# Performance work log

Measured on AMD Instinct MI355X. Metric: run time of the kernel, lower is better.

The kernel has to match this reference:

```python
import jax, jax.numpy as jnp
import numpy as np

N_NODES = 20000
N_EDGES = 320000
L = 512   # input feature dim (size_dict['small'][0])
D = 256   # hidden dim (feat_channel), heads=1 so head_dim = 256
C = 2     # n_classes


def setup_inputs() -> dict:
    key = jax.random.key(0)
    ks = jax.random.split(key, 18)
    s = 0.02
    inp = {
        "x": jax.random.normal(ks[0], (N_NODES, L), jnp.float32),
        "edge_index": jax.random.randint(ks[1], (2, N_EDGES), 0, N_NODES, dtype=jnp.int32),
        "label": 1,
        # TransformerConv(L, D, heads=1): query/key/value + root skip projections
        "Wq": jax.random.normal(ks[2], (L, D), jnp.float32) * s,
        "bq": jax.random.normal(ks[3], (D,), jnp.float32) * s,
        "Wk": jax.random.normal(ks[4], (L, D), jnp.float32) * s,
        "bk": jax.random.normal(ks[5], (D,), jnp.float32) * s,
        "Wv": jax.random.normal(ks[6], (L, D), jnp.float32) * s,
        "bv": jax.random.normal(ks[7], (D,), jnp.float32) * s,
        "Ws": jax.random.normal(ks[8], (L, D), jnp.float32) * s,
        "bs": jax.random.normal(ks[9], (D,), jnp.float32) * s,
        # GlobalAdaptPooling: tanh-MLP attention (heads = n_classes) + per-class classifier
        "Wa1": jax.random.normal(ks[10], (D, D), jnp.float32) * s,
        "ba1": jax.random.normal(ks[11], (D,), jnp.float32) * s,
        "Wa2": jax.random.normal(ks[12], (D, C), jnp.float32) * s,
        "ba2": jax.random.normal(ks[13], (C,), jnp.float32) * s,
        "Wc": jax.random.normal(ks[14], (C, D), jnp.float32) * s,
        "bc": jax.random.normal(ks[15], (C,), jnp.float32) * s,
    }
    return inp


def _forward(x, edge_index, label, Wq, bq, Wk, bk, Wv, bv, Ws, bs, Wa1, ba1, Wa2, ba2, Wc, bc):
    n = x.shape[0]
    src = edge_index[0]  # message source j
    dst = edge_index[1]  # message target i
    # --- TransformerConv (heads=1, concat, root_weight=True) ---
    q = x @ Wq + bq                      # [N, D]
    k = x @ Wk + bk
    v = x @ Wv + bv
    score = jnp.sum(q[dst] * k[src], axis=-1) / jnp.sqrt(jnp.float32(D))  # [E]
    # segment softmax over incoming edges of each target node
    m = jax.ops.segment_max(score, dst, num_segments=n)
    e = jnp.exp(score - m[dst])
    den = jax.ops.segment_sum(e, dst, num_segments=n)
    alpha = e / den[dst]                 # [E]
    agg = jax.ops.segment_sum(alpha[:, None] * v[src], dst, num_segments=n)  # [N, D]
    h = agg + x @ Ws + bs
    # --- act: GELU (torch exact/erf) ---
    h = jax.nn.gelu(h, approximate=False)
    # --- GlobalAdaptPooling: node attention with n_classes heads ---
    scores = jnp.tanh(h @ Wa1 + ba1) @ Wa2 + ba2      # [N, C]
    attn = jax.nn.softmax(scores, axis=0)             # softmax over nodes
    M = attn.T @ h                                    # [C, D] per-class bag embedding
    logits = (jnp.sum(M * Wc, axis=1) + bc)[None, :]  # [1, C]
    Y_prob = jax.nn.softmax(logits, axis=1)
    A = attn[:, label]                                # [N] attention for target class
    return logits, Y_prob, A


def reference(x, edge_index, label, Wq, bq, Wk, bk, Wv, bv, Ws, bs, Wa1, ba1, Wa2, ba2, Wc, bc):
    return _forward(x, edge_index, label, Wq, bq, Wk, bk, Wv, bv, Ws, bs, Wa1, ba1, Wa2, ba2, Wc, bc)
```

## Files before the change

kernel.cpp:

```cpp
#include <hip/hip_runtime.h>
#include <hip/hip_bf16.h>
#include <math.h>

typedef float f32x4_t __attribute__((ext_vector_type(4)));
typedef float f32x2_t __attribute__((ext_vector_type(2)));
typedef __bf16 bf16x8_t __attribute__((ext_vector_type(8)));

__device__ __forceinline__ float bf2f(unsigned int u){
  union { float f; unsigned int i; } x; x.i = u << 16; return x.f;
}
__device__ __forceinline__ unsigned short f2bf(float f){
  unsigned int x = __float_as_uint(f);
  unsigned int r = (x + 0x7fffu + ((x >> 16) & 1u)) >> 16;
  return (unsigned short)r;
}
__device__ __forceinline__ void unp8s(uint4 w, float* f, float s){
  f[0] = bf2f(w.x & 0xffffu) * s; f[1] = bf2f(w.x >> 16) * s;
  f[2] = bf2f(w.y & 0xffffu) * s; f[3] = bf2f(w.y >> 16) * s;
  f[4] = bf2f(w.z & 0xffffu) * s; f[5] = bf2f(w.z >> 16) * s;
  f[6] = bf2f(w.w & 0xffffu) * s; f[7] = bf2f(w.w >> 16) * s;
}
__device__ __forceinline__ void unpf8(unsigned int w, float* f){
  f32x2_t lo = __builtin_amdgcn_cvt_pk_f32_fp8(w, false);
  f32x2_t hi = __builtin_amdgcn_cvt_pk_f32_fp8(w, true);
  f[0] = lo[0]; f[1] = lo[1]; f[2] = hi[0]; f[3] = hi[1];
}

#define GLOAD16(gsrc, ldst) \
  __builtin_amdgcn_global_load_lds((const __attribute__((address_space(1))) unsigned int*)(gsrc), \
                                   (__attribute__((address_space(3))) unsigned int*)(ldst), 16, 0, 0)

__global__ void pack_weights(const float* __restrict__ Wq, const float* __restrict__ Wk,
                             const float* __restrict__ Wv, const float* __restrict__ Ws,
                             const float* __restrict__ bq, const float* __restrict__ bk,
                             const float* __restrict__ bv, const float* __restrict__ bs,
                             unsigned short* __restrict__ wcatT, float* __restrict__ bcat){
  int idx = blockIdx.x * 256 + threadIdx.x;
  if (idx < 1024 * 512){
    int c = idx >> 9, k = idx & 511;
    int sel = c >> 8, cc = c & 255;
    const float* W = (sel == 0) ? Wq : (sel == 1) ? Wk : (sel == 2) ? Wv : Ws;
    wcatT[idx] = f2bf(W[k * 256 + cc]);
  }
  if (idx < 1024){
    int sel = idx >> 8, cc = idx & 255;
    const float* B = (sel == 0) ? bq : (sel == 1) ? bk : (sel == 2) ? bv : bs;
    bcat[idx] = B[cc];
  }
}

__global__ void pack_wa1(const float* __restrict__ Wa1, unsigned short* __restrict__ wa1T){
  int idx = blockIdx.x * 256 + threadIdx.x;
  int c = idx >> 8, k = idx & 255;
  wa1T[idx] = f2bf(Wa1[k * 256 + c]);
}

__global__ void convert_x(const float* __restrict__ x, unsigned short* __restrict__ xbf, int n4){
  int i = blockIdx.x * 256 + threadIdx.x;
  if (i < n4){
    float4 v = reinterpret_cast<const float4*>(x)[i];
    ushort4 o;
    o.x = f2bf(v.x); o.y = f2bf(v.y); o.z = f2bf(v.z); o.w = f2bf(v.w);
    reinterpret_cast<ushort4*>(xbf)[i] = o;
  }
}

__global__ __launch_bounds__(256) void gemm_qkvs(const unsigned short* __restrict__ xbf,
                                                 const unsigned short* __restrict__ wcatT,
                                                 const float* __restrict__ bcat,
                                                 unsigned short* __restrict__ qkvs, int n_nodes){
  __shared__ __align__(16) unsigned short As[128 * 32];
  __shared__ __align__(16) unsigned short Bs[128 * 32];
  const int tid = threadIdx.x;
  const int lane = tid & 63, wave = tid >> 6;
  const int wm = wave >> 1, wn = wave & 1;
  const int m0 = blockIdx.y * 128, n0 = blockIdx.x * 128;
  const int lrow = lane >> 2;
  const int lcol = (lane & 3) * 8;
  const int rA0 = min(m0 + wave * 16 + lrow, n_nodes - 1);
  const int rA1 = min(m0 + (wave + 4) * 16 + lrow, n_nodes - 1);
  const int rB0 = n0 + wave * 16 + lrow;
  const int rB1 = n0 + (wave + 4) * 16 + lrow;
  const int r = lane & 15, ko = (lane >> 4) * 8;
  f32x4_t acc[4][4] = {};
  for (int k0 = 0; k0 < 512; k0 += 32){
    GLOAD16(xbf   + (size_t)rA0 * 512 + k0 + lcol, &As[wave * 512]);
    GLOAD16(xbf   + (size_t)rA1 * 512 + k0 + lcol, &As[(wave + 4) * 512]);
    GLOAD16(wcatT + (size_t)rB0 * 512 + k0 + lcol, &Bs[wave * 512]);
    GLOAD16(wcatT + (size_t)rB1 * 512 + k0 + lcol, &Bs[(wave + 4) * 512]);
    __syncthreads();
    bf16x8_t a[4], b[4];
    #pragma unroll
    for (int mi = 0; mi < 4; mi++)
      a[mi] = *reinterpret_cast<const bf16x8_t*>(&As[(wm * 64 + mi * 16 + r) * 32 + ko]);
    #pragma unroll
    for (int ni = 0; ni < 4; ni++)
      b[ni] = *reinterpret_cast<const bf16x8_t*>(&Bs[(wn * 64 + ni * 16 + r) * 32 + ko]);
    #pragma unroll
    for (int mi = 0; mi < 4; mi++)
      #pragma unroll
      for (int ni = 0; ni < 4; ni++)
        acc[mi][ni] = __builtin_amdgcn_mfma_f32_16x16x32_bf16(a[mi], b[ni], acc[mi][ni], 0, 0, 0);
    __syncthreads();
  }
  const int rg = (lane >> 4) * 4;
  #pragma unroll
  for (int ni = 0; ni < 4; ni++){
    int gcol = n0 + wn * 64 + ni * 16 + r;
    float bb = bcat[gcol];
    #pragma unroll
    for (int mi = 0; mi < 4; mi++){
      #pragma unroll
      for (int j = 0; j < 4; j++){
        int grow = m0 + wm * 64 + mi * 16 + rg + j;
        if (grow < n_nodes)
          qkvs[(size_t)grow * 1024 + gcol] = f2bf(acc[mi][ni][j] + bb);
      }
    }
  }
}

__global__ void pack_kv8(const unsigned short* __restrict__ qkvs, unsigned char* __restrict__ kv8, int n){
  int idx = blockIdx.x * 256 + threadIdx.x;
  if (idx >= n * 64) return;
  int node = idx >> 6, part = idx & 63;
  const unsigned short* src = qkvs + (size_t)node * 1024 + 256 + part * 8;
  uint4 w = *reinterpret_cast<const uint4*>(src);
  float f[8]; unp8s(w, f, 1.0f);
  int lo = 0, hi = 0;
  lo = __builtin_amdgcn_cvt_pk_fp8_f32(f[0], f[1], lo, false);
  lo = __builtin_amdgcn_cvt_pk_fp8_f32(f[2], f[3], lo, true);
  hi = __builtin_amdgcn_cvt_pk_fp8_f32(f[4], f[5], hi, false);
  hi = __builtin_amdgcn_cvt_pk_fp8_f32(f[6], f[7], hi, true);
  uint2 o; o.x = (unsigned int)lo; o.y = (unsigned int)hi;
  *reinterpret_cast<uint2*>(kv8 + (size_t)node * 512 + part * 8) = o;
}

__global__ void degree_hist(const int* __restrict__ ei, int* __restrict__ deg, int ne){
  int i = blockIdx.x * 256 + threadIdx.x;
  if (i < ne) atomicAdd(&deg[ei[ne + i]], 1);
}

__global__ void scan_deg(const int* __restrict__ deg, int* __restrict__ rowstart, int n, int ne){
  __shared__ int sm[1024];
  int tid = threadIdx.x;
  int per = (n + 1023) / 1024;
  int start = tid * per;
  int sum = 0;
  for (int i = 0; i < per; i++){
    int idx = start + i;
    sum += (idx < n) ? deg[idx] : 0;
  }
  sm[tid] = sum; __syncthreads();
  for (int off = 1; off < 1024; off <<= 1){
    int t = (tid >= off) ? sm[tid - off] : 0;
    __syncthreads();
    sm[tid] += t;
    __syncthreads();
  }
  int run = sm[tid] - sum;
  for (int i = 0; i < per; i++){
    int idx = start + i;
    if (idx < n){
      rowstart[idx] = run;
      run += deg[idx];
    }
  }
  if (tid == 0) rowstart[n] = ne;
}

__global__ void scatter_edges(const int* __restrict__ ei, const int* __restrict__ rowstart,
                              int* __restrict__ cursor, int* __restrict__ csrsrc, int ne){
  int i = blockIdx.x * 256 + threadIdx.x;
  if (i < ne){
    int d = ei[ne + i];
    int pos = atomicAdd(&cursor[d], 1);
    csrsrc[rowstart[d] + pos] = ei[i] << 9;
  }
}

__global__ __launch_bounds__(256) void edge_attn(const unsigned short* __restrict__ qkvs,
                                                 const unsigned char* __restrict__ kv8,
                                                 const int* __restrict__ rowstart,
                                                 const int* __restrict__ csrsrc,
                                                 unsigned short* __restrict__ hbf, int n_nodes){
  const int tid = threadIdx.x;
  const int lane = tid & 63, wave = tid >> 6;
  const int g = lane >> 4, t = lane & 15;
  const int node = blockIdx.x * 16 + wave * 4 + g;
  const bool active = node < n_nodes;
  const int nd = active ? node : 0;
  const float qs = 0.0625f * 1.44269504088896340736f;
  float q[16];
  {
    const unsigned short* qp = qkvs + (size_t)nd * 1024 + t * 16;
    uint4 w0 = *reinterpret_cast<const uint4*>(qp);
    uint4 w1 = *reinterpret_cast<const uint4*>(qp + 8);
    unp8s(w0, q, qs); unp8s(w1, q + 8, qs);
  }
  int rs = rowstart[nd];
  int re = active ? rowstart[nd + 1] : rs;
  float m = -1e30f, den = 0.f;
  float acc[16];
  #pragma unroll
  for (int j = 0; j < 16; j++) acc[j] = 0.f;
  for (int i = rs; i < re; i++){
    int soff = csrsrc[i];
    const unsigned char* kb = kv8 + (size_t)soff + t * 16;
    uint4 kw = *reinterpret_cast<const uint4*>(kb);
    float kf[16];
    unpf8(kw.x, kf); unpf8(kw.y, kf + 4); unpf8(kw.z, kf + 8); unpf8(kw.w, kf + 12);
    float s = 0.f;
    #pragma unroll
    for (int j = 0; j < 16; j++) s = fmaf(q[j], kf[j], s);
    s += __shfl_xor(s, 1); s += __shfl_xor(s, 2);
    s += __shfl_xor(s, 4); s += __shfl_xor(s, 8);
    uint4 vw = *reinterpret_cast<const uint4*>(kb + 256);
    float vf[16];
    unpf8(vw.x, vf); unpf8(vw.y, vf + 4); unpf8(vw.z, vf + 8); unpf8(vw.w, vf + 12);
    if (s > m){
      float sc = exp2f(m - s);
      den = den * sc + 1.0f;
      #pragma unroll
      for (int j = 0; j < 16; j++) acc[j] = fmaf(acc[j], sc, vf[j]);
      m = s;
    } else {
      float e = exp2f(s - m);
      den += e;
      #pragma unroll
      for (int j = 0; j < 16; j++) acc[j] = fmaf(e, vf[j], acc[j]);
    }
  }
  float inv = (den > 0.f) ? 1.f / den : 0.f;
  const unsigned short* sp = qkvs + (size_t)nd * 1024 + 768 + t * 16;
  uint4 s0 = *reinterpret_cast<const uint4*>(sp);
  uint4 s1 = *reinterpret_cast<const uint4*>(sp + 8);
  float sf[16]; unp8s(s0, sf, 1.0f); unp8s(s1, sf + 8, 1.0f);
  const float inv_sqrt2 = 0.70710678118654752f;
  unsigned int o[8];
  #pragma unroll
  for (int j = 0; j < 8; j++){
    float h0 = acc[2 * j] * inv + sf[2 * j];
    float h1 = acc[2 * j + 1] * inv + sf[2 * j + 1];
    h0 = 0.5f * h0 * (1.f + erff(h0 * inv_sqrt2));
    h1 = 0.5f * h1 * (1.f + erff(h1 * inv_sqrt2));
    o[j] = (unsigned int)f2bf(h0) | ((unsigned int)f2bf(h1) << 16);
  }
  if (active){
    uint4* dst = reinterpret_cast<uint4*>(hbf + (size_t)node * 256 + t * 16);
    dst[0] = make_uint4(o[0], o[1], o[2], o[3]);
    dst[1] = make_uint4(o[4], o[5], o[6], o[7]);
  }
}

__global__ __launch_bounds__(256) void mlp_mfma(const unsigned short* __restrict__ hbf,
                                                const unsigned short* __restrict__ wa1T,
                                                const float* __restrict__ ba1,
                                                const float* __restrict__ Wa2,
                                                const float* __restrict__ ba2,
                                                float* __restrict__ s2, int n_nodes){
  __shared__ __align__(16) unsigned short As[64 * 72];
  __shared__ float s2s[64][2];
  const int tid = threadIdx.x;
  const int lane = tid & 63, wave = tid >> 6;
  const int m0 = blockIdx.x * 64;
  const int c0 = wave * 64;
  const int r = lane & 15, rg = (lane >> 4) * 4;
  if (tid < 128) s2s[tid >> 1][tid & 1] = 0.f;
  f32x4_t acc[4][4] = {};
  for (int k0 = 0; k0 < 256; k0 += 64){
    int arow = tid >> 2, akc = (tid & 3) * 16;
    uint4 a0v = make_uint4(0,0,0,0), a1v = make_uint4(0,0,0,0);
    if (m0 + arow < n_nodes){
      const unsigned short* src = hbf + (size_t)(m0 + arow) * 256 + k0 + akc;
      a0v = *reinterpret_cast<const uint4*>(src);
      a1v = *reinterpret_cast<const uint4*>(src + 8);
    }
    *reinterpret_cast<uint4*>(&As[arow * 72 + akc]) = a0v;
    *reinterpret_cast<uint4*>(&As[arow * 72 + akc + 8]) = a1v;
    __syncthreads();
    #pragma unroll
    for (int kk = 0; kk < 2; kk++){
      int kg = kk * 32 + (lane >> 4) * 8;
      bf16x8_t a[4], b[4];
      #pragma unroll
      for (int mi = 0; mi < 4; mi++)
        a[mi] = *reinterpret_cast<const bf16x8_t*>(&As[(mi * 16 + r) * 72 + kg]);
      #pragma unroll
      for (int ni = 0; ni < 4; ni++)
        b[ni] = *reinterpret_cast<const bf16x8_t*>(wa1T + (size_t)(c0 + ni * 16 + r) * 256 + k0 + kg);
      #pragma unroll
      for (int mi = 0; mi < 4; mi++)
        #pragma unroll
        for (int ni = 0; ni < 4; ni++)
          acc[mi][ni] = __builtin_amdgcn_mfma_f32_16x16x32_bf16(a[mi], b[ni], acc[mi][ni], 0, 0, 0);
    }
    __syncthreads();
  }
  float w20[4], w21[4], b1c[4];
  #pragma unroll
  for (int ni = 0; ni < 4; ni++){
    int col = c0 + ni * 16 + r;
    w20[ni] = Wa2[col * 2]; w21[ni] = Wa2[col * 2 + 1]; b1c[ni] = ba1[col];
  }
  #pragma unroll
  for (int mi = 0; mi < 4; mi++){
    #pragma unroll
    for (int j = 0; j < 4; j++){
      float t0 = 0.f, t1 = 0.f;
      #pragma unroll
      for (int ni = 0; ni < 4; ni++){
        float t = tanhf(acc[mi][ni][j] + b1c[ni]);
        t0 += t * w20[ni]; t1 += t * w21[ni];
      }
      t0 += __shfl_xor(t0, 1); t0 += __shfl_xor(t0, 2);
      t0 += __shfl_xor(t0, 4); t0 += __shfl_xor(t0, 8);
      t1 += __shfl_xor(t1, 1); t1 += __shfl_xor(t1, 2);
      t1 += __shfl_xor(t1, 4); t1 += __shfl_xor(t1, 8);
      if (r == 0){
        int row = mi * 16 + rg + j;
        atomicAdd(&s2s[row][0], t0);
        atomicAdd(&s2s[row][1], t1);
      }
    }
  }
  __syncthreads();
  if (tid < 128){
    int row = tid >> 1, c = tid & 1;
    int node = m0 + row;
    if (node < n_nodes) s2[node * 2 + c] = s2s[row][c] + ba2[c];
  }
}

__global__ void col_reduce(const float* __restrict__ s2, float* __restrict__ red, int n){
  __shared__ float sm[1024];
  __shared__ float mshare[2];
  int tid = threadIdx.x;
  float mx0 = -INFINITY, mx1 = -INFINITY;
  for (int i = tid; i < n; i += 1024){
    mx0 = fmaxf(mx0, s2[2 * i]);
    mx1 = fmaxf(mx1, s2[2 * i + 1]);
  }
  sm[tid] = mx0; __syncthreads();
  for (int off = 512; off > 0; off >>= 1){
    if (tid < off) sm[tid] = fmaxf(sm[tid], sm[tid + off]);
    __syncthreads();
  }
  if (tid == 0) mshare[0] = sm[0];
  __syncthreads();
  sm[tid] = mx1; __syncthreads();
  for (int off = 512; off > 0; off >>= 1){
    if (tid < off) sm[tid] = fmaxf(sm[tid], sm[tid + off]);
    __syncthreads();
  }
  if (tid == 0) mshare[1] = sm[0];
  __syncthreads();
  float m0 = mshare[0], m1 = mshare[1];
  float s0 = 0.f, s1 = 0.f;
  for (int i = tid; i < n; i += 1024){
    s0 += expf(s2[2 * i] - m0);
    s1 += expf(s2[2 * i + 1] - m1);
  }
  sm[tid] = s0; __syncthreads();
  for (int off = 512; off > 0; off >>= 1){
    if (tid < off) sm[tid] += sm[tid + off];
    __syncthreads();
  }
  float den0 = sm[0];
  __syncthreads();
  sm[tid] = s1; __syncthreads();
  for (int off = 512; off > 0; off >>= 1){
    if (tid < off) sm[tid] += sm[tid + off];
    __syncthreads();
  }
  if (tid == 0){
    red[0] = m0; red[1] = m1; red[2] = den0; red[3] = sm[0];
  }
}

__global__ __launch_bounds__(256) void attn_M(const float* __restrict__ s2, const float* __restrict__ red,
                                              const unsigned short* __restrict__ hbf, const int* __restrict__ label,
                                              float* __restrict__ Mbuf, float* __restrict__ outA, int n){
  __shared__ float a0s[256], a1s[256];
  int tid = threadIdx.x;
  int n0 = blockIdx.x * 256;
  int node = n0 + tid;
  float m0 = red[0], m1 = red[1];
  float i0 = 1.f / red[2], i1 = 1.f / red[3];
  float a0 = 0.f, a1 = 0.f;
  if (node < n){
    a0 = expf(s2[2 * node] - m0) * i0;
    a1 = expf(s2[2 * node + 1] - m1) * i1;
    outA[node] = (label[0] == 0) ? a0 : a1;
  }
  a0s[tid] = a0; a1s[tid] = a1;
  __syncthreads();
  int d = tid;
  float M0 = 0.f, M1 = 0.f;
  int cnt = min(256, n - n0);
  for (int i = 0; i < cnt; i++){
    float hv = bf2f((unsigned int)hbf[(size_t)(n0 + i) * 256 + d]);
    M0 += a0s[i] * hv;
    M1 += a1s[i] * hv;
  }
  atomicAdd(&Mbuf[d], M0);
  atomicAdd(&Mbuf[256 + d], M1);
}

__global__ void final_k(const float* __restrict__ Mbuf, const float* __restrict__ Wc,
                        const float* __restrict__ bc, float* __restrict__ out){
  __shared__ float sm[256];
  __shared__ float l0s;
  int tid = threadIdx.x;
  float p0 = Mbuf[tid] * Wc[tid];
  float p1 = Mbuf[256 + tid] * Wc[256 + tid];
  sm[tid] = p0; __syncthreads();
  for (int off = 128; off > 0; off >>= 1){
    if (tid < off) sm[tid] += sm[tid + off];
    __syncthreads();
  }
  if (tid == 0) l0s = sm[0];
  __syncthreads();
  sm[tid] = p1; __syncthreads();
  for (int off = 128; off > 0; off >>= 1){
    if (tid < off) sm[tid] += sm[tid + off];
    __syncthreads();
  }
  if (tid == 0){
    float l0 = l0s + bc[0];
    float l1 = sm[0] + bc[1];
    out[0] = l0; out[1] = l1;
    float mx = fmaxf(l0, l1);
    float e0 = expf(l0 - mx), e1 = expf(l1 - mx);
    float inv = 1.f / (e0 + e1);
    out[2] = e0 * inv; out[3] = e1 * inv;
  }
}

extern "C" void kernel_launch(void* const* d_in, const int* in_sizes, int n_in,
                              void* d_out, int out_size, void* d_ws, size_t ws_size,
                              hipStream_t stream) {
  const float* x   = (const float*)d_in[0];
  const int*   ei  = (const int*)d_in[1];
  const int*   lab = (const int*)d_in[2];
  const float* Wq  = (const float*)d_in[3];
  const float* bq  = (const float*)d_in[4];
  const float* Wk  = (const float*)d_in[5];
  const float* bk  = (const float*)d_in[6];
  const float* Wv  = (const float*)d_in[7];
  const float* bv  = (const float*)d_in[8];
  const float* Ws  = (const float*)d_in[9];
  const float* bs  = (const float*)d_in[10];
  const float* Wa1 = (const float*)d_in[11];
  const float* ba1 = (const float*)d_in[12];
  const float* Wa2 = (const float*)d_in[13];
  const float* ba2 = (const float*)d_in[14];
  const float* Wc  = (const float*)d_in[15];
  const float* bc  = (const float*)d_in[16];
  float* out = (float*)d_out;

  const int n  = in_sizes[0] / 512;
  const int ne = in_sizes[1] / 2;

  char* ws = (char*)d_ws;
  size_t off = 0;
  auto take = [&](size_t bytes){ size_t r = off; off += (bytes + 255) & ~(size_t)255; return r; };
  unsigned short* xbf    = (unsigned short*)(ws + take((size_t)n * 512 * 2));
  unsigned short* wcatT  = (unsigned short*)(ws + take((size_t)1024 * 512 * 2));
  float*          bcat   = (float*)(ws + take(1024 * 4));
  unsigned short* qkvs   = (unsigned short*)(ws + take((size_t)n * 1024 * 2));
  unsigned char*  kv8    = (unsigned char*)(ws + take((size_t)n * 512));
  unsigned short* hbf    = (unsigned short*)(ws + take((size_t)n * 256 * 2));
  unsigned short* wa1T   = (unsigned short*)(ws + take((size_t)256 * 256 * 2));
  float*          s2     = (float*)(ws + take((size_t)n * 2 * 4));
  size_t zoff = off;
  int*            deg    = (int*)(ws + take((size_t)n * 4));
  int*            cursor = (int*)(ws + take((size_t)n * 4));
  float*          Mbuf   = (float*)(ws + take(512 * 4));
  size_t zlen = off - zoff;
  int*            rowst  = (int*)(ws + take((size_t)(n + 1) * 4));
  int*            csrsrc = (int*)(ws + take((size_t)ne * 4));
  float*          red    = (float*)(ws + take(4 * 4));

  hipMemsetAsync(ws + zoff, 0, zlen, stream);

  pack_weights<<<(1024 * 512 + 255) / 256, 256, 0, stream>>>(Wq, Wk, Wv, Ws, bq, bk, bv, bs, wcatT, bcat);
  pack_wa1<<<256, 256, 0, stream>>>(Wa1, wa1T);
  convert_x<<<(n * 512 / 4 + 255) / 256, 256, 0, stream>>>(x, xbf, n * 512 / 4);
  dim3 ggrid(8, (n + 127) / 128);
  gemm_qkvs<<<ggrid, 256, 0, stream>>>(xbf, wcatT, bcat, qkvs, n);
  pack_kv8<<<(n * 64 + 255) / 256, 256, 0, stream>>>(qkvs, kv8, n);
  degree_hist<<<(ne + 255) / 256, 256, 0, stream>>>(ei, deg, ne);
  scan_deg<<<1, 1024, 0, stream>>>(deg, rowst, n, ne);
  scatter_edges<<<(ne + 255) / 256, 256, 0, stream>>>(ei, rowst, cursor, csrsrc, ne);
  edge_attn<<<(n + 15) / 16, 256, 0, stream>>>(qkvs, kv8, rowst, csrsrc, hbf, n);
  mlp_mfma<<<(n + 63) / 64, 256, 0, stream>>>(hbf, wa1T, ba1, Wa2, ba2, s2, n);
  col_reduce<<<1, 1024, 0, stream>>>(s2, red, n);
  attn_M<<<(n + 255) / 256, 256, 0, stream>>>(s2, red, hbf, lab, Mbuf, out + 4, n);
  final_k<<<1, 256, 0, stream>>>(Mbuf, Wc, bc, out);
  (void)ws_size; (void)out_size; (void)n_in;
}
```

Baseline: 226.2 us.

## Fuse x conversion and KV fp8 packing into QKVS GEMM with staged epilogue

Drops the separate convert_x and pack_kv8 kernels. The GEMM now reads fp32 x, converts it to bf16 in registers and stores it to LDS, and its epilogue writes Q and S as separate bf16 arrays and K/V directly as fp8. Output tiles are staged through shared memory so global stores are coalesced, and the blocks are remapped to a 1D grid with n-block-major grouping. This removes two launches, the xbf round trip and the full qkvs intermediate. In exchange, the A operand is now loaded synchronously through registers instead of via global_load_lds, which could expose more load latency.

```diff
diff --git a/kernel.cpp b/kernel.cpp
--- a/kernel.cpp
+++ b/kernel.cpp
@@ -13,6 +13,9 @@
   unsigned int x = __float_as_uint(f);
   unsigned int r = (x + 0x7fffu + ((x >> 16) & 1u)) >> 16;
   return (unsigned short)r;
+}
+__device__ __forceinline__ unsigned int pk2bf(float a, float b){
+  return (unsigned int)f2bf(a) | ((unsigned int)f2bf(b) << 16);
 }
 __device__ __forceinline__ void unp8s(uint4 w, float* f, float s){
   f[0] = bf2f(w.x & 0xffffu) * s; f[1] = bf2f(w.x >> 16) * s;
@@ -55,39 +58,44 @@
   wa1T[idx] = f2bf(Wa1[k * 256 + c]);
 }
 
-__global__ void convert_x(const float* __restrict__ x, unsigned short* __restrict__ xbf, int n4){
-  int i = blockIdx.x * 256 + threadIdx.x;
-  if (i < n4){
-    float4 v = reinterpret_cast<const float4*>(x)[i];
-    ushort4 o;
-    o.x = f2bf(v.x); o.y = f2bf(v.y); o.z = f2bf(v.z); o.w = f2bf(v.w);
-    reinterpret_cast<ushort4*>(xbf)[i] = o;
-  }
-}
-
-__global__ __launch_bounds__(256) void gemm_qkvs(const unsigned short* __restrict__ xbf,
+__global__ __launch_bounds__(256) void gemm_qkvs(const float* __restrict__ x,
                                                  const unsigned short* __restrict__ wcatT,
                                                  const float* __restrict__ bcat,
-                                                 unsigned short* __restrict__ qkvs, int n_nodes){
-  __shared__ __align__(16) unsigned short As[128 * 32];
-  __shared__ __align__(16) unsigned short Bs[128 * 32];
+                                                 unsigned short* __restrict__ qbf,
+                                                 unsigned short* __restrict__ sbf,
+                                                 unsigned char* __restrict__ kv8,
+                                                 int n_nodes, int mblocks){
+  __shared__ __align__(16) unsigned char smem[128 * 272];
+  unsigned short* As = (unsigned short*)smem;
+  unsigned short* Bs = (unsigned short*)(smem + 8192);
   const int tid = threadIdx.x;
   const int lane = tid & 63, wave = tid >> 6;
   const int wm = wave >> 1, wn = wave & 1;
-  const int m0 = blockIdx.y * 128, n0 = blockIdx.x * 128;
-  const int lrow = lane >> 2;
-  const int lcol = (lane & 3) * 8;
-  const int rA0 = min(m0 + wave * 16 + lrow, n_nodes - 1);
-  const int rA1 = min(m0 + (wave + 4) * 16 + lrow, n_nodes - 1);
-  const int rB0 = n0 + wave * 16 + lrow;
-  const int rB1 = n0 + (wave + 4) * 16 + lrow;
-  const int r = lane & 15, ko = (lane >> 4) * 8;
+  const int g = (blockIdx.x & 7) * mblocks + (blockIdx.x >> 3);
+  const int m_blk = g >> 3, n_blk = g & 7;
+  const int m0 = m_blk * 128, n0 = n_blk * 128;
+  const int arow = tid >> 1;
+  const int acol = (tid & 1) * 16;
+  const float* aptr = x + (size_t)min(m0 + arow, n_nodes - 1) * 512 + acol;
+  unsigned short* adst = &As[arow * 32 + acol];
+  const int brow = n0 + wave * 16 + (lane >> 2);
+  const int bcol = (lane & 3) * 8;
+  const int r = lane & 15, ko = (lane >> 4) * 8, ng = lane >> 4;
   f32x4_t acc[4][4] = {};
   for (int k0 = 0; k0 < 512; k0 += 32){
-    GLOAD16(xbf   + (size_t)rA0 * 512 + k0 + lcol, &As[wave * 512]);
-    GLOAD16(xbf   + (size_t)rA1 * 512 + k0 + lcol, &As[(wave + 4) * 512]);
-    GLOAD16(wcatT + (size_t)rB0 * 512 + k0 + lcol, &Bs[wave * 512]);
-    GLOAD16(wcatT + (size_t)rB1 * 512 + k0 + lcol, &Bs[(wave + 4) * 512]);
+    GLOAD16(wcatT + (size_t)brow * 512 + k0 + bcol, &Bs[wave * 512]);
+    GLOAD16(wcatT + (size_t)(brow + 64) * 512 + k0 + bcol, &Bs[(wave + 4) * 512]);
+    float4 f0 = *reinterpret_cast<const float4*>(aptr + k0);
+    float4 f1 = *reinterpret_cast<const float4*>(aptr + k0 + 4);
+    float4 f2 = *reinterpret_cast<const float4*>(aptr + k0 + 8);
+    float4 f3 = *reinterpret_cast<const float4*>(aptr + k0 + 12);
+    uint4 o0, o1;
+    o0.x = pk2bf(f0.x, f0.y); o0.y = pk2bf(f0.z, f0.w);
+    o0.z = pk2bf(f1.x, f1.y); o0.w = pk2bf(f1.z, f1.w);
+    o1.x = pk2bf(f2.x, f2.y); o1.y = pk2bf(f2.z, f2.w);
+    o1.z = pk2bf(f3.x, f3.y); o1.w = pk2bf(f3.z, f3.w);
+    *reinterpret_cast<uint4*>(adst) = o0;
+    *reinterpret_cast<uint4*>(adst + 8) = o1;
     __syncthreads();
     bf16x8_t a[4], b[4];
     #pragma unroll
@@ -100,40 +108,65 @@
     for (int mi = 0; mi < 4; mi++)
       #pragma unroll
       for (int ni = 0; ni < 4; ni++)
-        acc[mi][ni] = __builtin_amdgcn_mfma_f32_16x16x32_bf16(a[mi], b[ni], acc[mi][ni], 0, 0, 0);
-    __syncthreads();
-  }
-  const int rg = (lane >> 4) * 4;
-  #pragma unroll
-  for (int ni = 0; ni < 4; ni++){
-    int gcol = n0 + wn * 64 + ni * 16 + r;
-    float bb = bcat[gcol];
+        acc[mi][ni] = __builtin_amdgcn_mfma_f32_16x16x32_bf16(b[ni], a[mi], acc[mi][ni], 0, 0, 0);
+    __syncthreads();
+  }
+  const bool isQ = (n_blk < 2), isS = (n_blk >= 6);
+  if (isQ || isS){
+    unsigned short* St = (unsigned short*)smem;
     #pragma unroll
     for (int mi = 0; mi < 4; mi++){
       #pragma unroll
-      for (int j = 0; j < 4; j++){
-        int grow = m0 + wm * 64 + mi * 16 + rg + j;
-        if (grow < n_nodes)
-          qkvs[(size_t)grow * 1024 + gcol] = f2bf(acc[mi][ni][j] + bb);
+      for (int ni = 0; ni < 4; ni++){
+        int ml = wm * 64 + mi * 16 + r;
+        int nl = wn * 64 + ni * 16 + ng * 4;
+        float4 bb = *reinterpret_cast<const float4*>(&bcat[n0 + nl]);
+        uint2 w;
+        w.x = pk2bf(acc[mi][ni][0] + bb.x, acc[mi][ni][1] + bb.y);
+        w.y = pk2bf(acc[mi][ni][2] + bb.z, acc[mi][ni][3] + bb.w);
+        *reinterpret_cast<uint2*>(&St[ml * 136 + nl]) = w;
       }
     }
-  }
-}
-
-__global__ void pack_kv8(const unsigned short* __restrict__ qkvs, unsigned char* __restrict__ kv8, int n){
-  int idx = blockIdx.x * 256 + threadIdx.x;
-  if (idx >= n * 64) return;
-  int node = idx >> 6, part = idx & 63;
-  const unsigned short* src = qkvs + (size_t)node * 1024 + 256 + part * 8;
-  uint4 w = *reinterpret_cast<const uint4*>(src);
-  float f[8]; unp8s(w, f, 1.0f);
-  int lo = 0, hi = 0;
-  lo = __builtin_amdgcn_cvt_pk_fp8_f32(f[0], f[1], lo, false);
-  lo = __builtin_amdgcn_cvt_pk_fp8_f32(f[2], f[3], lo, true);
-  hi = __builtin_amdgcn_cvt_pk_fp8_f32(f[4], f[5], hi, false);
-  hi = __builtin_amdgcn_cvt_pk_fp8_f32(f[6], f[7], hi, true);
-  uint2 o; o.x = (unsigned int)lo; o.y = (unsigned int)hi;
-  *reinterpret_cast<uint2*>(kv8 + (size_t)node * 512 + part * 8) = o;
+    __syncthreads();
+    unsigned short* outp = isQ ? qbf : sbf;
+    const int colhalf = isQ ? n_blk : (n_blk - 6);
+    #pragma unroll
+    for (int it = 0; it < 8; it++){
+      int t = it * 256 + tid;
+      int row = t >> 4, seg = (t & 15) * 8;
+      int node = m0 + row;
+      if (node < n_nodes){
+        uint4 v = *reinterpret_cast<const uint4*>(&St[row * 136 + seg]);
+        *reinterpret_cast<uint4*>(outp + (size_t)node * 256 + colhalf * 128 + seg) = v;
+      }
+    }
+  } else {
+    unsigned char* St = smem;
+    #pragma unroll
+    for (int mi = 0; mi < 4; mi++){
+      #pragma unroll
+      for (int ni = 0; ni < 4; ni++){
+        int ml = wm * 64 + mi * 16 + r;
+        int nl = wn * 64 + ni * 16 + ng * 4;
+        float4 bb = *reinterpret_cast<const float4*>(&bcat[n0 + nl]);
+        int u = 0;
+        u = __builtin_amdgcn_cvt_pk_fp8_f32(acc[mi][ni][0] + bb.x, acc[mi][ni][1] + bb.y, u, false);
+        u = __builtin_amdgcn_cvt_pk_fp8_f32(acc[mi][ni][2] + bb.z, acc[mi][ni][3] + bb.w, u, true);
+        *reinterpret_cast<unsigned int*>(&St[ml * 144 + nl]) = (unsigned int)u;
+      }
+    }
+    __syncthreads();
+    #pragma unroll
+    for (int it = 0; it < 4; it++){
+      int t = it * 256 + tid;
+      int row = t >> 3, seg = (t & 7) * 16;
+      int node = m0 + row;
+      if (node < n_nodes){
+        uint4 v = *reinterpret_cast<const uint4*>(&St[row * 144 + seg]);
+        *reinterpret_cast<uint4*>(kv8 + (size_t)node * 512 + (n_blk - 2) * 128 + seg) = v;
+      }
+    }
+  }
 }
 
 __global__ void degree_hist(const int* __restrict__ ei, int* __restrict__ deg, int ne){
@@ -179,7 +212,8 @@
   }
 }
 
-__global__ __launch_bounds__(256) void edge_attn(const unsigned short* __restrict__ qkvs,
+__global__ __launch_bounds__(256) void edge_attn(const unsigned short* __restrict__ qbf,
+                                                 const unsigned short* __restrict__ sbf,
                                                  const unsigned char* __restrict__ kv8,
                                                  const int* __restrict__ rowstart,
                                                  const int* __restrict__ csrsrc,
@@ -193,7 +227,7 @@
   const float qs = 0.0625f * 1.44269504088896340736f;
   float q[16];
   {
-    const unsigned short* qp = qkvs + (size_t)nd * 1024 + t * 16;
+    const unsigned short* qp = qbf + (size_t)nd * 256 + t * 16;
     uint4 w0 = *reinterpret_cast<const uint4*>(qp);
     uint4 w1 = *reinterpret_cast<const uint4*>(qp + 8);
     unp8s(w0, q, qs); unp8s(w1, q + 8, qs);
@@ -232,7 +266,7 @@
     }
   }
   float inv = (den > 0.f) ? 1.f / den : 0.f;
-  const unsigned short* sp = qkvs + (size_t)nd * 1024 + 768 + t * 16;
+  const unsigned short* sp = sbf + (size_t)nd * 256 + t * 16;
   uint4 s0 = *reinterpret_cast<const uint4*>(sp);
   uint4 s1 = *reinterpret_cast<const uint4*>(sp + 8);
   float sf[16]; unp8s(s0, sf, 1.0f); unp8s(s1, sf + 8, 1.0f);
@@ -465,10 +499,10 @@
   char* ws = (char*)d_ws;
   size_t off = 0;
   auto take = [&](size_t bytes){ size_t r = off; off += (bytes + 255) & ~(size_t)255; return r; };
-  unsigned short* xbf    = (unsigned short*)(ws + take((size_t)n * 512 * 2));
   unsigned short* wcatT  = (unsigned short*)(ws + take((size_t)1024 * 512 * 2));
   float*          bcat   = (float*)(ws + take(1024 * 4));
-  unsigned short* qkvs   = (unsigned short*)(ws + take((size_t)n * 1024 * 2));
+  unsigned short* qbf    = (unsigned short*)(ws + take((size_t)n * 256 * 2));
+  unsigned short* sbf    = (unsigned short*)(ws + take((size_t)n * 256 * 2));
   unsigned char*  kv8    = (unsigned char*)(ws + take((size_t)n * 512));
   unsigned short* hbf    = (unsigned short*)(ws + take((size_t)n * 256 * 2));
   unsigned short* wa1T   = (unsigned short*)(ws + take((size_t)256 * 256 * 2));
@@ -486,14 +520,12 @@
 
   pack_weights<<<(1024 * 512 + 255) / 256, 256, 0, stream>>>(Wq, Wk, Wv, Ws, bq, bk, bv, bs, wcatT, bcat);
   pack_wa1<<<256, 256, 0, stream>>>(Wa1, wa1T);
-  convert_x<<<(n * 512 / 4 + 255) / 256, 256, 0, stream>>>(x, xbf, n * 512 / 4);
-  dim3 ggrid(8, (n + 127) / 128);
-  gemm_qkvs<<<ggrid, 256, 0, stream>>>(xbf, wcatT, bcat, qkvs, n);
-  pack_kv8<<<(n * 64 + 255) / 256, 256, 0, stream>>>(qkvs, kv8, n);
+  const int mblocks = (n + 127) / 128;
+  gemm_qkvs<<<8 * mblocks, 256, 0, stream>>>(x, wcatT, bcat, qbf, sbf, kv8, n, mblocks);
   degree_hist<<<(ne + 255) / 256, 256, 0, stream>>>(ei, deg, ne);
   scan_deg<<<1, 1024, 0, stream>>>(deg, rowst, n, ne);
   scatter_edges<<<(ne + 255) / 256, 256, 0, stream>>>(ei, rowst, cursor, csrsrc, ne);
-  edge_attn<<<(n + 15) / 16, 256, 0, stream>>>(qkvs, kv8, rowst, csrsrc, hbf, n);
+  edge_attn<<<(n + 15) / 16, 256, 0, stream>>>(qbf, sbf, kv8, rowst, csrsrc, hbf, n);
   mlp_mfma<<<(n + 63) / 64, 256, 0, stream>>>(hbf, wa1T, ba1, Wa2, ba2, s2, n);
   col_reduce<<<1, 1024, 0, stream>>>(s2, red, n);
   attn_M<<<(n + 255) / 256, 256, 0, stream>>>(s2, red, hbf, lab, Mbuf, out + 4, n);
```

Result: faster. 218.9 us (-3.2%).
